# Performance work log

Hardware: AMD Instinct MI355X
Metric: run time of the kernel (lower is better)

## Reference

```python
import jax, jax.numpy as jnp
import numpy as np

NI = 512
HEADS = 8
DH = NI // HEADS  # 64 = attn_chans
EPS = 1e-5

def _ln(x, g, b):
    mu = jnp.mean(x, axis=-1, keepdims=True)
    var = jnp.var(x, axis=-1, keepdims=True)
    return (x - mu) * jax.lax.rsqrt(var + EPS) * g + b

def setup_inputs() -> dict:
    key = jax.random.key(0)
    ks = jax.random.split(key, 5)
    n, c, h, w = 8, NI, 32, 32
    return {
        "x": jax.random.normal(ks[0], (n, c, h, w), jnp.float32),
        "query_x": jax.random.normal(ks[1], (n, c, h, w), jnp.float32),
        "q_ln_g": jnp.ones((c,), jnp.float32),
        "q_ln_b": jnp.zeros((c,), jnp.float32),
        "q_w": jax.random.normal(ks[2], (c, c), jnp.float32) / np.sqrt(c),
        "q_b": jnp.zeros((c,), jnp.float32),
        "kv_ln_g": jnp.ones((c,), jnp.float32),
        "kv_ln_b": jnp.zeros((c,), jnp.float32),
        "kv_w": jax.random.normal(ks[3], (c, 2 * c), jnp.float32) / np.sqrt(c),
        "kv_b": jnp.zeros((2 * c,), jnp.float32),
        "proj_w": jax.random.normal(ks[4], (c, c), jnp.float32) / np.sqrt(c),
        "proj_b": jnp.zeros((c,), jnp.float32),
    }

def reference(x, query_x, q_ln_g, q_ln_b, q_w, q_b, kv_ln_g, kv_ln_b, kv_w, kv_b, proj_w, proj_b):
    n, c, h, w = x.shape
    s = h * w
    xs = x.reshape(n, c, s).transpose(0, 2, 1)        # (n, s, c)
    qx = query_x.reshape(n, c, s).transpose(0, 2, 1)  # (n, s, c)
    q_proj = _ln(qx, q_ln_g, q_ln_b) @ q_w + q_b        # (n, s, c)
    kv = _ln(xs, kv_ln_g, kv_ln_b) @ kv_w + kv_b        # (n, s, 2c)
    cat = jnp.concatenate([q_proj, kv], axis=-1)        # (n, s, 3c)
    # rearrange 'n s (h d3)' with h=HEADS, d3 = 3*DH, then chunk into q,k,v
    cat = cat.reshape(n, s, HEADS, 3 * DH).transpose(0, 2, 1, 3)  # (n, H, s, 3d)
    q, k, v = jnp.split(cat, 3, axis=-1)                # each (n, H, s, d)
    scale = jnp.sqrt(jnp.asarray(DH, q.dtype))          # sqrt(ni/nheads)
    scores = jnp.einsum('nhqd,nhkd->nhqk', q, k) / scale
    attn = jax.nn.softmax(scores, axis=-1)
    o = jnp.einsum('nhqk,nhkd->nhqd', attn, v)          # (n, H, s, d)
    o = o.transpose(0, 2, 1, 3).reshape(n, s, c)        # (n, s, c)
    o = o @ proj_w + proj_b
    return o.transpose(0, 2, 1).reshape(n, c, h, w)
```

## Files before the change

kernel.cpp:

```cpp
#include <hip/hip_runtime.h>
#include <math.h>

namespace {

constexpr int S = 1024;
constexpr int C = 512;
constexpr int NBATCH = 8;
constexpr int RTOT = NBATCH * S;
constexpr int HEADS = 8;
constexpr int DH = 64;

typedef __attribute__((ext_vector_type(8))) short bf16x8;
typedef __attribute__((ext_vector_type(4))) float f32x4;
typedef unsigned short u16;
typedef unsigned int u32;

__device__ __forceinline__ u16 f2bf(float x) {
  union { float f; u32 u; } v; v.f = x;
  u32 r = v.u + 0x7FFF + ((v.u >> 16) & 1);
  return (u16)(r >> 16);
}
__device__ __forceinline__ float bf2f(u16 b) {
  union { u32 u; float f; } v; v.u = (u32)b << 16; return v.f;
}
__device__ __forceinline__ void gl_lds16(const void* g, void* l) {
  auto gp = (const __attribute__((address_space(1))) u32*)g;
  auto lp = (__attribute__((address_space(3))) u32*)l;
  __builtin_amdgcn_global_load_lds(gp, lp, 16, 0, 0);
}

__global__ void ln_fused(const float* __restrict__ x, const float* __restrict__ qx,
                         const float* __restrict__ gx, const float* __restrict__ bx,
                         const float* __restrict__ gq, const float* __restrict__ bq,
                         u16* __restrict__ Xkv, u16* __restrict__ Xq) {
  __shared__ float Ssum[8][32], Ssq[8][32];
  __shared__ float mu_s[32], rs_s[32];
  __shared__ float T[32][65];
  int t = threadIdx.x;
  int si0 = blockIdx.x * 32;
  int isq = blockIdx.y & 1, n = blockIdx.y >> 1;
  const float* in = isq ? qx : x;
  const float* g  = isq ? gq : gx;
  const float* be = isq ? bq : bx;
  u16* out = isq ? Xq : Xkv;

  {
    int sl = t & 31, cg = t >> 5;
    const float* p = in + ((size_t)n * C + cg * 64) * S + si0 + sl;
    float s = 0.f, sq = 0.f;
#pragma unroll 8
    for (int c = 0; c < 64; c++) { float v = p[(size_t)c * S]; s += v; sq += v * v; }
    Ssum[cg][sl] = s; Ssq[cg][sl] = sq;
  }
  __syncthreads();
  if (t < 32) {
    float ss = 0.f, q2 = 0.f;
#pragma unroll
    for (int i = 0; i < 8; i++) { ss += Ssum[i][t]; q2 += Ssq[i][t]; }
    float m = ss * (1.0f / C);
    float var = q2 * (1.0f / C) - m * m;
    mu_s[t] = m; rs_s[t] = rsqrtf(var + 1e-5f);
  }
  __syncthreads();

  int si4 = (t & 7) * 4, cl = t >> 3;
  float4 mu4 = *(const float4*)&mu_s[si4];
  float4 rs4 = *(const float4*)&rs_s[si4];
  int wsl = t >> 3, wc8 = (t & 7) * 8;

  for (int c0 = 0; c0 < C; c0 += 64) {
#pragma unroll
    for (int i = 0; i < 2; i++) {
      int c = c0 + cl + i * 32;
      float4 v = *(const float4*)&in[((size_t)n * C + c) * S + si0 + si4];
      float gg = g[c], bb = be[c];
      T[si4 + 0][cl + i * 32] = (v.x - mu4.x) * rs4.x * gg + bb;
      T[si4 + 1][cl + i * 32] = (v.y - mu4.y) * rs4.y * gg + bb;
      T[si4 + 2][cl + i * 32] = (v.z - mu4.z) * rs4.z * gg + bb;
      T[si4 + 3][cl + i * 32] = (v.w - mu4.w) * rs4.w * gg + bb;
    }
    __syncthreads();
    u16 pk[8];
#pragma unroll
    for (int j = 0; j < 8; j++) pk[j] = f2bf(T[wsl][wc8 + j]);
    *(uint4*)&out[((size_t)(n * S + si0 + wsl)) * C + c0 + wc8] = *(const uint4*)pk;
    __syncthreads();
  }
}

__global__ void prep_w(const float* __restrict__ qw, const float* __restrict__ kvw,
                       const float* __restrict__ pw,
                       u16* __restrict__ Wtq, u16* __restrict__ Wtkv,
                       u16* __restrict__ Wph, u16* __restrict__ Wpl) {
  int z = blockIdx.z;
  int N = (z == 1) ? 1024 : 512;
  int col0 = blockIdx.y * 64;
  if (col0 >= N) return;
  int k0 = blockIdx.x * 64;
  const float* W = (z == 0) ? qw : (z == 1) ? kvw : pw;
  __shared__ float T[64][65];
  int t = threadIdx.x;
  int kl = t >> 4, c4 = (t & 15) * 4;
#pragma unroll
  for (int i = 0; i < 4; i++) {
    float4 v = *(const float4*)&W[(size_t)(k0 + kl + i * 16) * N + col0 + c4];
    T[kl + i * 16][c4 + 0] = v.x; T[kl + i * 16][c4 + 1] = v.y;
    T[kl + i * 16][c4 + 2] = v.z; T[kl + i * 16][c4 + 3] = v.w;
  }
  __syncthreads();
#pragma unroll
  for (int p = 0; p < 2; p++) {
    int cl = (t >> 3) + p * 32, k8 = (t & 7) * 8;
    u16 hi[8], lo[8];
#pragma unroll
    for (int j = 0; j < 8; j++) {
      float f = T[k8 + j][cl];
      u16 hv = f2bf(f);
      hi[j] = hv;
      lo[j] = f2bf(f - bf2f(hv));
    }
    size_t o = (size_t)(col0 + cl) * 512 + k0 + k8;
    if (z == 0) *(uint4*)&Wtq[o] = *(const uint4*)hi;
    else if (z == 1) *(uint4*)&Wtkv[o] = *(const uint4*)hi;
    else { *(uint4*)&Wph[o] = *(const uint4*)hi; *(uint4*)&Wpl[o] = *(const uint4*)lo; }
  }
}

__global__ __launch_bounds__(256, 4) void gemm_qkv(
    const u16* __restrict__ Xq, const u16* __restrict__ Xkv,
    const u16* __restrict__ Wtq, const u16* __restrict__ Wtkv,
    const float* __restrict__ q_b, const float* __restrict__ kv_b,
    u16* __restrict__ Qb, u16* __restrict__ Kb, u16* __restrict__ Vt) {
  __shared__ __attribute__((aligned(16))) u16 As[128 * 64];
  __shared__ __attribute__((aligned(16))) u16 Bs[128 * 64];
  int t = threadIdx.x, wid = t >> 6, lane = t & 63, lr = lane & 15, lg = lane >> 4;
  int colb = blockIdx.x;
  const u16* A; const u16* Wt; const float* bias; int ch0;
  if (colb < 4) { A = Xq;  Wt = Wtq  + (size_t)colb * 128 * 512;       bias = q_b  + colb * 128;       ch0 = colb * 128; }
  else          { A = Xkv; Wt = Wtkv + (size_t)(colb - 4) * 128 * 512; bias = kv_b + (colb - 4) * 128; ch0 = 512 + (colb - 4) * 128; }
  int row0 = blockIdx.y * 128;
  int wr = wid >> 1, wc = wid & 1;
  f32x4 acc[4][4];
#pragma unroll
  for (int m = 0; m < 4; m++)
#pragma unroll
    for (int n = 0; n < 4; n++) acc[m][n] = (f32x4){0.f, 0.f, 0.f, 0.f};

  for (int k0 = 0; k0 < 512; k0 += 64) {
    __syncthreads();
#pragma unroll
    for (int it = 0; it < 4; it++) {
      int chunk = (wid * 4 + it) * 64 + lane;
      int r = chunk >> 3, sg = chunk & 7;
      gl_lds16(A + (size_t)(row0 + r) * 512 + k0 + ((sg ^ (r & 7)) * 8),
               (char*)As + (size_t)chunk * 16);
    }
#pragma unroll
    for (int it = 0; it < 4; it++) {
      int chunk = (wid * 4 + it) * 64 + lane;
      int r = chunk >> 3, sg = chunk & 7;
      gl_lds16(Wt + (size_t)r * 512 + k0 + ((sg ^ (r & 7)) * 8),
               (char*)Bs + (size_t)chunk * 16);
    }
    __syncthreads();
#pragma unroll
    for (int kk = 0; kk < 2; kk++) {
      bf16x8 bfr[4];
#pragma unroll
      for (int n = 0; n < 4; n++) {
        int col = wc * 64 + n * 16 + lr;
        bfr[n] = *(const bf16x8*)((const char*)Bs + col * 128 + (((kk * 4 + lg) ^ (col & 7)) << 4));
      }
#pragma unroll
      for (int m = 0; m < 4; m++) {
        int row = wr * 64 + m * 16 + lr;
        bf16x8 af = *(const bf16x8*)((const char*)As + row * 128 + (((kk * 4 + lg) ^ (row & 7)) << 4));
#pragma unroll
        for (int n = 0; n < 4; n++)
          acc[m][n] = __builtin_amdgcn_mfma_f32_16x16x32_bf16(af, bfr[n], acc[m][n], 0, 0, 0);
      }
    }
  }
#pragma unroll
  for (int m = 0; m < 4; m++)
#pragma unroll
    for (int n = 0; n < 4; n++) {
      int colg = wc * 64 + n * 16 + lr;
      int ch = ch0 + colg;
      int h = ch / 192, role = (ch >> 6) % 3, d = ch & 63;
      float bs = bias[colg];
      float qsc = (role == 0) ? 0.18033688f : 1.0f;
      int growb = row0 + wr * 64 + m * 16 + lg * 4;
      int nn = growb >> 10, ssi0 = growb & (S - 1);
      size_t nh = (size_t)(nn * HEADS + h);
      if (role == 2) {
        u16 pk[4];
#pragma unroll
        for (int r = 0; r < 4; r++) pk[r] = f2bf(acc[m][n][r] + bs);
        *(uint2*)&Vt[(nh * DH + d) * S + ssi0] = *(const uint2*)pk;
      } else {
        u16* dst = (role == 0) ? Qb : Kb;
#pragma unroll
        for (int r = 0; r < 4; r++)
          dst[(nh * S + ssi0 + r) * DH + d] = f2bf((acc[m][n][r] + bs) * qsc);
      }
    }
}

__global__ __launch_bounds__(256) void gemm_proj(
    const u16* __restrict__ Aob, const u16* __restrict__ Wh, const u16* __restrict__ Wl,
    const float* __restrict__ bias, float* __restrict__ out) {
  __shared__ __attribute__((aligned(16))) u16 As[128 * 64];
  __shared__ __attribute__((aligned(16))) u16 Bh[64 * 64];
  __shared__ __attribute__((aligned(16))) u16 Bl[64 * 64];
  int t = threadIdx.x, wid = t >> 6, lane = t & 63, lr = lane & 15, lg = lane >> 4;
  int ch0 = blockIdx.x * 64, row0 = blockIdx.y * 128;
  int wc = wid & 1, wr = wid >> 1;
  f32x4 acc[2][4];
#pragma unroll
  for (int m = 0; m < 2; m++)
#pragma unroll
    for (int n = 0; n < 4; n++) acc[m][n] = (f32x4){0.f, 0.f, 0.f, 0.f};

  for (int k0 = 0; k0 < 512; k0 += 64) {
    __syncthreads();
#pragma unroll
    for (int it = 0; it < 4; it++) {
      int idx = (wid * 4 + it) * 64 + lane;
      int r = idx >> 3, sg = idx & 7;
      gl_lds16(Aob + (size_t)(row0 + r) * 512 + k0 + ((sg ^ (r & 7)) * 8),
               (char*)As + (wid * 4 + it) * 1024);
    }
#pragma unroll
    for (int it = 0; it < 2; it++) {
      int idx = (wid * 2 + it) * 64 + lane;
      int r = idx >> 3, sg = idx & 7;
      size_t go = (size_t)(ch0 + r) * 512 + k0 + ((sg ^ (r & 7)) * 8);
      gl_lds16(Wh + go, (char*)Bh + (wid * 2 + it) * 1024);
      gl_lds16(Wl + go, (char*)Bl + (wid * 2 + it) * 1024);
    }
    __syncthreads();
#pragma unroll
    for (int kk = 0; kk < 2; kk++) {
      bf16x8 ar[4];
#pragma unroll
      for (int n = 0; n < 4; n++) {
        int row = wr * 64 + n * 16 + lr;
        ar[n] = *(const bf16x8*)((const char*)As + row * 128 + (((kk * 4 + lg) ^ (row & 7)) << 4));
      }
#pragma unroll
      for (int m = 0; m < 2; m++) {
        int ch = wc * 32 + m * 16 + lr;
        bf16x8 bh = *(const bf16x8*)((const char*)Bh + ch * 128 + (((kk * 4 + lg) ^ (ch & 7)) << 4));
        bf16x8 bl = *(const bf16x8*)((const char*)Bl + ch * 128 + (((kk * 4 + lg) ^ (ch & 7)) << 4));
#pragma unroll
        for (int n = 0; n < 4; n++) {
          acc[m][n] = __builtin_amdgcn_mfma_f32_16x16x32_bf16(bh, ar[n], acc[m][n], 0, 0, 0);
          acc[m][n] = __builtin_amdgcn_mfma_f32_16x16x32_bf16(bl, ar[n], acc[m][n], 0, 0, 0);
        }
      }
    }
  }
#pragma unroll
  for (int m = 0; m < 2; m++)
#pragma unroll
    for (int n = 0; n < 4; n++) {
      int rowg = row0 + wr * 64 + n * 16 + lr;
      int nn = rowg >> 10, ssi = rowg & (S - 1);
#pragma unroll
      for (int r = 0; r < 4; r++) {
        int ch = ch0 + wc * 32 + m * 16 + lg * 4 + r;
        out[((size_t)nn * C + ch) * S + ssi] = acc[m][n][r] + bias[ch];
      }
    }
}

constexpr int KVB = 64;

__global__ __launch_bounds__(256, 4) void attn_kernel(
    const u16* __restrict__ Qbf, const u16* __restrict__ Kbf,
    const u16* __restrict__ Vtb, u16* __restrict__ Obf) {
  __shared__ __attribute__((aligned(16))) u16 Ks[2][KVB * DH];
  __shared__ __attribute__((aligned(16))) u16 Vs[2][DH * KVB];
  __shared__ __attribute__((aligned(16))) u16 Ps[4][16 * KVB];

  int tid = threadIdx.x;
  int wave = tid >> 6, lane = tid & 63;
  int lr = lane & 15, lg = lane >> 4;
  int w = (blockIdx.x & 7) * 128 + (blockIdx.x >> 3);
  int qt = w & 15, nh = w >> 4;
  const u16* Qg = Qbf + (size_t)nh * S * DH;
  const u16* Kg = Kbf + (size_t)nh * S * DH;
  const u16* Vg = Vtb + (size_t)nh * DH * S;

  int qrow = qt * 64 + wave * 16 + lr;
  bf16x8 qf0 = *(const bf16x8*)(Qg + (size_t)qrow * DH + lg * 8);
  bf16x8 qf1 = *(const bf16x8*)(Qg + (size_t)qrow * DH + lg * 8 + 32);

  bf16x8 ones;
#pragma unroll
  for (int i = 0; i < 8; i++) ones[i] = (short)0x3F80;

  f32x4 oacc[4], lacc;
#pragma unroll
  for (int dt = 0; dt < 4; dt++) oacc[dt] = (f32x4){0.f, 0.f, 0.f, 0.f};
  lacc = (f32x4){0.f, 0.f, 0.f, 0.f};
  float m_run = -1e30f;

  char* Pw = (char*)&Ps[wave][0];
  int e0i = tid, e1i = tid + 256;
  int r0 = e0i >> 3, sg0 = e0i & 7, r1 = e1i >> 3, sg1 = e1i & 7;
  char* kd0 = (char*)&Ks[0][0] + (e0i & ~63) * 16;
  char* kd1 = (char*)&Ks[0][0] + (e1i & ~63) * 16;
  char* vd0 = (char*)&Vs[0][0] + (e0i & ~63) * 16;
  char* vd1 = (char*)&Vs[0][0] + (e1i & ~63) * 16;

#define STAGE(kb, b)                                                             \
  do {                                                                           \
    gl_lds16(Kg + (size_t)((kb) * KVB + r0) * 64 + ((sg0 ^ (r0 & 7)) * 8),       \
             kd0 + (b) * (KVB * DH * 2));                                        \
    gl_lds16(Kg + (size_t)((kb) * KVB + r1) * 64 + ((sg1 ^ (r1 & 7)) * 8),       \
             kd1 + (b) * (KVB * DH * 2));                                        \
    gl_lds16(Vg + (size_t)r0 * S + (kb) * KVB + ((sg0 ^ (r0 & 7)) * 8),          \
             vd0 + (b) * (KVB * DH * 2));                                        \
    gl_lds16(Vg + (size_t)r1 * S + (kb) * KVB + ((sg1 ^ (r1 & 7)) * 8),          \
             vd1 + (b) * (KVB * DH * 2));                                        \
  } while (0)

  STAGE(0, 0);

  for (int kb = 0; kb < S / KVB; kb++) {
    int cur = kb & 1;
    __syncthreads();
    if (kb + 1 < S / KVB) STAGE(kb + 1, cur ^ 1);

    const char* Kc = (const char*)&Ks[cur][0];
    const char* Vc = (const char*)&Vs[cur][0];

    f32x4 sc[4];
#pragma unroll
    for (int t = 0; t < 4; t++) {
      int key = t * 16 + lr;
      const char* kr = Kc + key * 128;
      bf16x8 kf0 = *(const bf16x8*)(kr + ((lg * 16) ^ ((lr & 7) << 4)));
      bf16x8 kf1 = *(const bf16x8*)(kr + (((lg * 16) + 64) ^ ((lr & 7) << 4)));
      f32x4 z = (f32x4){0.f, 0.f, 0.f, 0.f};
      z = __builtin_amdgcn_mfma_f32_16x16x32_bf16(kf0, qf0, z, 0, 0, 0);
      sc[t] = __builtin_amdgcn_mfma_f32_16x16x32_bf16(kf1, qf1, z, 0, 0, 0);
    }

    float pmax = -1e30f;
#pragma unroll
    for (int t = 0; t < 4; t++) {
      float a = fmaxf(fmaxf(sc[t][0], sc[t][1]), fmaxf(sc[t][2], sc[t][3]));
      pmax = fmaxf(pmax, a);
    }
    pmax = fmaxf(pmax, __shfl_xor(pmax, 16));
    pmax = fmaxf(pmax, __shfl_xor(pmax, 32));

    if (!__all(pmax <= m_run + 11.5f)) {
      float mnew = fmaxf(m_run, pmax);
      float corr = exp2f(m_run - mnew);
      m_run = mnew;
      float cr[4];
#pragma unroll
      for (int r = 0; r < 4; r++) cr[r] = __shfl(corr, lg * 4 + r);
#pragma unroll
      for (int r = 0; r < 4; r++) lacc[r] *= cr[r];
#pragma unroll
      for (int dt = 0; dt < 4; dt++)
#pragma unroll
        for (int r = 0; r < 4; r++) oacc[dt][r] *= cr[r];
    }

#pragma unroll
    for (int t = 0; t < 4; t++) {
      float e0 = exp2f(sc[t][0] - m_run);
      float e1 = exp2f(sc[t][1] - m_run);
      float e2 = exp2f(sc[t][2] - m_run);
      float e3 = exp2f(sc[t][3] - m_run);
      uint2 pw;
      pw.x = (u32)f2bf(e0) | ((u32)f2bf(e1) << 16);
      pw.y = (u32)f2bf(e2) | ((u32)f2bf(e3) << 16);
      *(uint2*)(Pw + lr * 128 + ((t * 32 + lg * 8) ^ ((lr & 7) << 4))) = pw;
    }

#pragma unroll
    for (int kk = 0; kk < 2; kk++) {
      bf16x8 pf = *(const bf16x8*)(Pw + lr * 128 + ((kk * 64 + lg * 16) ^ ((lr & 7) << 4)));
      lacc = __builtin_amdgcn_mfma_f32_16x16x32_bf16(pf, ones, lacc, 0, 0, 0);
#pragma unroll
      for (int dt = 0; dt < 4; dt++) {
        int dd = dt * 16 + lr;
        bf16x8 vf = *(const bf16x8*)(Vc + dd * 128 + ((kk * 64 + lg * 16) ^ ((lr & 7) << 4)));
        oacc[dt] = __builtin_amdgcn_mfma_f32_16x16x32_bf16(pf, vf, oacc[dt], 0, 0, 0);
      }
    }
  }
#undef STAGE

  int n = nh >> 3, h = nh & 7;
  float lf[4];
#pragma unroll
  for (int r = 0; r < 4; r++) lf[r] = 1.0f / lacc[r];
#pragma unroll
  for (int dt = 0; dt < 4; dt++)
#pragma unroll
    for (int r = 0; r < 4; r++) {
      int q = qt * 64 + wave * 16 + lg * 4 + r;
      int d = dt * 16 + lr;
      Obf[((size_t)n * S + q) * C + h * DH + d] = f2bf(oacc[dt][r] * lf[r]);
    }
}

}

extern "C" void kernel_launch(void* const* d_in, const int* in_sizes, int n_in,
                              void* d_out, int out_size, void* d_ws, size_t ws_size,
                              hipStream_t stream) {
  const float* x       = (const float*)d_in[0];
  const float* qx      = (const float*)d_in[1];
  const float* q_ln_g  = (const float*)d_in[2];
  const float* q_ln_b  = (const float*)d_in[3];
  const float* q_w     = (const float*)d_in[4];
  const float* q_b     = (const float*)d_in[5];
  const float* kv_ln_g = (const float*)d_in[6];
  const float* kv_ln_b = (const float*)d_in[7];
  const float* kv_w    = (const float*)d_in[8];
  const float* kv_b    = (const float*)d_in[9];
  const float* proj_w  = (const float*)d_in[10];
  const float* proj_b  = (const float*)d_in[11];
  float* out = (float*)d_out;

  u16* u = (u16*)d_ws;
  u16* Xkv  = u;                u += (size_t)RTOT * C;
  u16* Xq   = u;                u += (size_t)RTOT * C;
  u16* Wtq  = u;                u += (size_t)C * C;
  u16* Wtkv = u;                u += (size_t)2 * C * C;
  u16* Wph  = u;                u += (size_t)C * C;
  u16* Wpl  = u;                u += (size_t)C * C;
  u16* Qb   = u;                u += (size_t)NBATCH * HEADS * S * DH;
  u16* Kb   = u;                u += (size_t)NBATCH * HEADS * S * DH;
  u16* Vt   = u;                u += (size_t)NBATCH * HEADS * S * DH;
  u16* Obf  = u;

  hipLaunchKernelGGL(ln_fused, dim3(S / 32, 2 * NBATCH), dim3(256), 0, stream,
                     x, qx, kv_ln_g, kv_ln_b, q_ln_g, q_ln_b, Xkv, Xq);
  hipLaunchKernelGGL(prep_w, dim3(8, 16, 3), dim3(256), 0, stream,
                     q_w, kv_w, proj_w, Wtq, Wtkv, Wph, Wpl);
  hipLaunchKernelGGL(gemm_qkv, dim3(12, RTOT / 128), dim3(256), 0, stream,
                     Xq, Xkv, Wtq, Wtkv, q_b, kv_b, Qb, Kb, Vt);
  hipLaunchKernelGGL(attn_kernel, dim3(1024), dim3(256), 0, stream,
                     Qb, Kb, Vt, Obf);
  hipLaunchKernelGGL(gemm_proj, dim3(C / 64, RTOT / 128), dim3(256), 0, stream,
                     Obf, Wph, Wpl, proj_b, out);
}
```

Before: 99.38 us.

## Rewrite attention with 32x32x16 MFMA, register-resident P via permlane swap

The attention kernel moves from 16x16x32 to 32x32x16 MFMA tiles, so each wave handles 32 query rows and each block 128, with the grid halved to 512 blocks. The softmax probabilities stay in registers: they are packed with v_cvt_pk_bf16_f32 and rearranged with v_permlane32_swap instead of a round trip through LDS. The row sum is computed with VALU adds rather than an MFMA against a ones vector. This removes LDS traffic and the extra MFMAs per tile, but raises register pressure (the launch-bounds occupancy hint is dropped) and halves the number of blocks available for parallelism.

```diff
diff --git a/kernel.cpp b/kernel.cpp
--- a/kernel.cpp
+++ b/kernel.cpp
@@ -12,6 +12,7 @@
 
 typedef __attribute__((ext_vector_type(8))) short bf16x8;
 typedef __attribute__((ext_vector_type(4))) float f32x4;
+typedef __attribute__((ext_vector_type(16))) float f32x16;
 typedef unsigned short u16;
 typedef unsigned int u32;
 
@@ -22,6 +23,11 @@
 }
 __device__ __forceinline__ float bf2f(u16 b) {
   union { u32 u; float f; } v; v.u = (u32)b << 16; return v.f;
+}
+__device__ __forceinline__ u32 cvtpk(float a, float b) {
+  u32 r;
+  asm("v_cvt_pk_bf16_f32 %0, %1, %2" : "=v"(r) : "v"(a), "v"(b));
+  return r;
 }
 __device__ __forceinline__ void gl_lds16(const void* g, void* l) {
   auto gp = (const __attribute__((address_space(1))) u32*)g;
@@ -277,37 +283,30 @@
 
 constexpr int KVB = 64;
 
-__global__ __launch_bounds__(256, 4) void attn_kernel(
+__global__ __launch_bounds__(256) void attn_kernel(
     const u16* __restrict__ Qbf, const u16* __restrict__ Kbf,
     const u16* __restrict__ Vtb, u16* __restrict__ Obf) {
   __shared__ __attribute__((aligned(16))) u16 Ks[2][KVB * DH];
   __shared__ __attribute__((aligned(16))) u16 Vs[2][DH * KVB];
-  __shared__ __attribute__((aligned(16))) u16 Ps[4][16 * KVB];
 
   int tid = threadIdx.x;
   int wave = tid >> 6, lane = tid & 63;
-  int lr = lane & 15, lg = lane >> 4;
-  int w = (blockIdx.x & 7) * 128 + (blockIdx.x >> 3);
-  int qt = w & 15, nh = w >> 4;
+  int lq = lane & 31, hi = lane >> 5;
+  int w = (blockIdx.x & 7) * 64 + (blockIdx.x >> 3);
+  int qt = w & 7, nh = w >> 3;
   const u16* Qg = Qbf + (size_t)nh * S * DH;
   const u16* Kg = Kbf + (size_t)nh * S * DH;
   const u16* Vg = Vtb + (size_t)nh * DH * S;
 
-  int qrow = qt * 64 + wave * 16 + lr;
-  bf16x8 qf0 = *(const bf16x8*)(Qg + (size_t)qrow * DH + lg * 8);
-  bf16x8 qf1 = *(const bf16x8*)(Qg + (size_t)qrow * DH + lg * 8 + 32);
-
-  bf16x8 ones;
-#pragma unroll
-  for (int i = 0; i < 8; i++) ones[i] = (short)0x3F80;
-
-  f32x4 oacc[4], lacc;
-#pragma unroll
-  for (int dt = 0; dt < 4; dt++) oacc[dt] = (f32x4){0.f, 0.f, 0.f, 0.f};
-  lacc = (f32x4){0.f, 0.f, 0.f, 0.f};
-  float m_run = -1e30f;
-
-  char* Pw = (char*)&Ps[wave][0];
+  int qrow = qt * 128 + wave * 32 + lq;
+  bf16x8 qf[4];
+#pragma unroll
+  for (int ks = 0; ks < 4; ks++)
+    qf[ks] = *(const bf16x8*)(Qg + (size_t)qrow * DH + ks * 16 + hi * 8);
+
+  f32x16 oa0 = {}, oa1 = {};
+  float m_run = -1e30f, l_run = 0.f;
+
   int e0i = tid, e1i = tid + 256;
   int r0 = e0i >> 3, sg0 = e0i & 7, r1 = e1i >> 3, sg1 = e1i & 7;
   char* kd0 = (char*)&Ks[0][0] + (e0i & ~63) * 16;
@@ -337,80 +336,86 @@
     const char* Kc = (const char*)&Ks[cur][0];
     const char* Vc = (const char*)&Vs[cur][0];
 
-    f32x4 sc[4];
-#pragma unroll
-    for (int t = 0; t < 4; t++) {
-      int key = t * 16 + lr;
-      const char* kr = Kc + key * 128;
-      bf16x8 kf0 = *(const bf16x8*)(kr + ((lg * 16) ^ ((lr & 7) << 4)));
-      bf16x8 kf1 = *(const bf16x8*)(kr + (((lg * 16) + 64) ^ ((lr & 7) << 4)));
-      f32x4 z = (f32x4){0.f, 0.f, 0.f, 0.f};
-      z = __builtin_amdgcn_mfma_f32_16x16x32_bf16(kf0, qf0, z, 0, 0, 0);
-      sc[t] = __builtin_amdgcn_mfma_f32_16x16x32_bf16(kf1, qf1, z, 0, 0, 0);
+    f32x16 sc0 = {}, sc1 = {};
+#pragma unroll
+    for (int ks = 0; ks < 4; ks++) {
+      int row0k = lq;
+      int row1k = 32 + lq;
+      int sg = ks * 2 + hi;
+      bf16x8 kf0 = *(const bf16x8*)(Kc + row0k * 128 + ((sg ^ (lq & 7)) << 4));
+      bf16x8 kf1 = *(const bf16x8*)(Kc + row1k * 128 + ((sg ^ (lq & 7)) << 4));
+      sc0 = __builtin_amdgcn_mfma_f32_32x32x16_bf16(kf0, qf[ks], sc0, 0, 0, 0);
+      sc1 = __builtin_amdgcn_mfma_f32_32x32x16_bf16(kf1, qf[ks], sc1, 0, 0, 0);
     }
 
     float pmax = -1e30f;
 #pragma unroll
-    for (int t = 0; t < 4; t++) {
-      float a = fmaxf(fmaxf(sc[t][0], sc[t][1]), fmaxf(sc[t][2], sc[t][3]));
-      pmax = fmaxf(pmax, a);
-    }
-    pmax = fmaxf(pmax, __shfl_xor(pmax, 16));
+    for (int r = 0; r < 16; r++) pmax = fmaxf(pmax, fmaxf(sc0[r], sc1[r]));
     pmax = fmaxf(pmax, __shfl_xor(pmax, 32));
 
     if (!__all(pmax <= m_run + 11.5f)) {
       float mnew = fmaxf(m_run, pmax);
       float corr = exp2f(m_run - mnew);
       m_run = mnew;
-      float cr[4];
-#pragma unroll
-      for (int r = 0; r < 4; r++) cr[r] = __shfl(corr, lg * 4 + r);
-#pragma unroll
-      for (int r = 0; r < 4; r++) lacc[r] *= cr[r];
-#pragma unroll
-      for (int dt = 0; dt < 4; dt++)
-#pragma unroll
-        for (int r = 0; r < 4; r++) oacc[dt][r] *= cr[r];
-    }
-
-#pragma unroll
-    for (int t = 0; t < 4; t++) {
-      float e0 = exp2f(sc[t][0] - m_run);
-      float e1 = exp2f(sc[t][1] - m_run);
-      float e2 = exp2f(sc[t][2] - m_run);
-      float e3 = exp2f(sc[t][3] - m_run);
-      uint2 pw;
-      pw.x = (u32)f2bf(e0) | ((u32)f2bf(e1) << 16);
-      pw.y = (u32)f2bf(e2) | ((u32)f2bf(e3) << 16);
-      *(uint2*)(Pw + lr * 128 + ((t * 32 + lg * 8) ^ ((lr & 7) << 4))) = pw;
-    }
-
-#pragma unroll
-    for (int kk = 0; kk < 2; kk++) {
-      bf16x8 pf = *(const bf16x8*)(Pw + lr * 128 + ((kk * 64 + lg * 16) ^ ((lr & 7) << 4)));
-      lacc = __builtin_amdgcn_mfma_f32_16x16x32_bf16(pf, ones, lacc, 0, 0, 0);
-#pragma unroll
-      for (int dt = 0; dt < 4; dt++) {
-        int dd = dt * 16 + lr;
-        bf16x8 vf = *(const bf16x8*)(Vc + dd * 128 + ((kk * 64 + lg * 16) ^ ((lr & 7) << 4)));
-        oacc[dt] = __builtin_amdgcn_mfma_f32_16x16x32_bf16(pf, vf, oacc[dt], 0, 0, 0);
-      }
+      l_run *= corr;
+#pragma unroll
+      for (int r = 0; r < 16; r++) { oa0[r] *= corr; oa1[r] *= corr; }
+    }
+
+    float psum = 0.f;
+#pragma unroll
+    for (int r = 0; r < 16; r++) { sc0[r] = exp2f(sc0[r] - m_run); psum += sc0[r]; }
+#pragma unroll
+    for (int r = 0; r < 16; r++) { sc1[r] = exp2f(sc1[r] - m_run); psum += sc1[r]; }
+    psum += __shfl_xor(psum, 32);
+    l_run += psum;
+
+    u32 c[16];
+    c[0]  = cvtpk(sc0[0],  sc0[1]);  c[1]  = cvtpk(sc0[2],  sc0[3]);
+    c[2]  = cvtpk(sc0[4],  sc0[5]);  c[3]  = cvtpk(sc0[6],  sc0[7]);
+    c[4]  = cvtpk(sc0[8],  sc0[9]);  c[5]  = cvtpk(sc0[10], sc0[11]);
+    c[6]  = cvtpk(sc0[12], sc0[13]); c[7]  = cvtpk(sc0[14], sc0[15]);
+    c[8]  = cvtpk(sc1[0],  sc1[1]);  c[9]  = cvtpk(sc1[2],  sc1[3]);
+    c[10] = cvtpk(sc1[4],  sc1[5]);  c[11] = cvtpk(sc1[6],  sc1[7]);
+    c[12] = cvtpk(sc1[8],  sc1[9]);  c[13] = cvtpk(sc1[10], sc1[11]);
+    c[14] = cvtpk(sc1[12], sc1[13]); c[15] = cvtpk(sc1[14], sc1[15]);
+    asm("v_permlane32_swap_b32 %0, %1" : "+v"(c[0]),  "+v"(c[2]));
+    asm("v_permlane32_swap_b32 %0, %1" : "+v"(c[1]),  "+v"(c[3]));
+    asm("v_permlane32_swap_b32 %0, %1" : "+v"(c[4]),  "+v"(c[6]));
+    asm("v_permlane32_swap_b32 %0, %1" : "+v"(c[5]),  "+v"(c[7]));
+    asm("v_permlane32_swap_b32 %0, %1" : "+v"(c[8]),  "+v"(c[10]));
+    asm("v_permlane32_swap_b32 %0, %1" : "+v"(c[9]),  "+v"(c[11]));
+    asm("v_permlane32_swap_b32 %0, %1" : "+v"(c[12]), "+v"(c[14]));
+    asm("v_permlane32_swap_b32 %0, %1" : "+v"(c[13]), "+v"(c[15]));
+
+#pragma unroll
+    for (int kk = 0; kk < 4; kk++) {
+      union { u32 u[4]; bf16x8 v; } pu;
+      pu.u[0] = c[kk * 4 + 0]; pu.u[1] = c[kk * 4 + 1];
+      pu.u[2] = c[kk * 4 + 2]; pu.u[3] = c[kk * 4 + 3];
+      int sg = kk * 2 + hi;
+      bf16x8 vf0 = *(const bf16x8*)(Vc + lq * 128 + ((sg ^ (lq & 7)) << 4));
+      bf16x8 vf1 = *(const bf16x8*)(Vc + (32 + lq) * 128 + ((sg ^ (lq & 7)) << 4));
+      oa0 = __builtin_amdgcn_mfma_f32_32x32x16_bf16(vf0, pu.v, oa0, 0, 0, 0);
+      oa1 = __builtin_amdgcn_mfma_f32_32x32x16_bf16(vf1, pu.v, oa1, 0, 0, 0);
     }
   }
 #undef STAGE
 
   int n = nh >> 3, h = nh & 7;
-  float lf[4];
-#pragma unroll
-  for (int r = 0; r < 4; r++) lf[r] = 1.0f / lacc[r];
-#pragma unroll
-  for (int dt = 0; dt < 4; dt++)
-#pragma unroll
-    for (int r = 0; r < 4; r++) {
-      int q = qt * 64 + wave * 16 + lg * 4 + r;
-      int d = dt * 16 + lr;
-      Obf[((size_t)n * S + q) * C + h * DH + d] = f2bf(oacc[dt][r] * lf[r]);
-    }
+  float lf = 1.0f / l_run;
+  u16* orow = Obf + ((size_t)n * S + qrow) * C + h * DH;
+#pragma unroll
+  for (int rq = 0; rq < 4; rq++) {
+    int d0 = rq * 8 + 4 * hi;
+    uint2 w0, w1;
+    w0.x = cvtpk(oa0[rq * 4 + 0] * lf, oa0[rq * 4 + 1] * lf);
+    w0.y = cvtpk(oa0[rq * 4 + 2] * lf, oa0[rq * 4 + 3] * lf);
+    w1.x = cvtpk(oa1[rq * 4 + 0] * lf, oa1[rq * 4 + 1] * lf);
+    w1.y = cvtpk(oa1[rq * 4 + 2] * lf, oa1[rq * 4 + 3] * lf);
+    *(uint2*)(orow + d0) = w0;
+    *(uint2*)(orow + 32 + d0) = w1;
+  }
 }
 
 }
@@ -450,7 +455,7 @@
                      q_w, kv_w, proj_w, Wtq, Wtkv, Wph, Wpl);
   hipLaunchKernelGGL(gemm_qkv, dim3(12, RTOT / 128), dim3(256), 0, stream,
                      Xq, Xkv, Wtq, Wtkv, q_b, kv_b, Qb, Kb, Vt);
-  hipLaunchKernelGGL(attn_kernel, dim3(1024), dim3(256), 0, stream,
+  hipLaunchKernelGGL(attn_kernel, dim3(512), dim3(256), 0, stream,
                      Qb, Kb, Vt, Obf);
   hipLaunchKernelGGL(gemm_proj, dim3(C / 64, RTOT / 128), dim3(256), 0, stream,
                      Obf, Wph, Wpl, proj_b, out);
```

New measurement: 98.53 us. About the same (-0.8%).
